# Kernel tuning notes

Measured on AMD Instinct MI355X. Metric: run time of the kernel, lower is better.

Reference implementation:

```python
import jax, jax.numpy as jnp
import numpy as np

N = 10000        # nodes
E = 320000       # edges (before self-loops)
F_IN = 128       # num_feature
H1, C1 = 16, 16  # GAT1: heads=16, out=16 -> concat 256
D = 256          # GAT2: heads=1, out=256
G = 64           # graphs in batch
L = 10           # num_label
NEG_SLOPE = 0.2


def setup_inputs() -> dict:
    key = jax.random.key(0)
    ks = jax.random.split(key, 13)
    sc = lambda f: 1.0 / np.sqrt(f)
    inp = {
        "x": jax.random.normal(ks[0], (N, F_IN), jnp.float32),
        "edge_index": jax.random.randint(ks[1], (2, E), 0, N, dtype=jnp.int32),
        "batch": jnp.sort(jax.random.randint(ks[2], (N,), 0, G, dtype=jnp.int32)),
        "W1": jax.random.normal(ks[3], (F_IN, H1 * C1), jnp.float32) * sc(F_IN),
        "a_src1": jax.random.normal(ks[4], (H1, C1), jnp.float32) * sc(C1),
        "a_dst1": jax.random.normal(ks[5], (H1, C1), jnp.float32) * sc(C1),
        "b1": jnp.zeros((H1 * C1,), jnp.float32),
        "W2": jax.random.normal(ks[6], (H1 * C1, D), jnp.float32) * sc(H1 * C1),
        "a_src2": jax.random.normal(ks[7], (1, D), jnp.float32) * sc(D),
        "a_dst2": jax.random.normal(ks[8], (1, D), jnp.float32) * sc(D),
        "b2": jnp.zeros((D,), jnp.float32),
        "lin_w": jax.random.normal(ks[9], (D, L), jnp.float32) * sc(D),
        "lin_b": jnp.zeros((L,), jnp.float32),
    }
    return inp


def _leaky(v):
    return jnp.where(v >= 0, v, NEG_SLOPE * v)


def gat_conv(x, src, dst, W, a_src, a_dst, bias, heads, ch):
    """PyG GATConv (eval mode): gather, leaky-relu logits, segment softmax over dst, scatter-add."""
    n = x.shape[0]
    h = (x @ W).reshape(n, heads, ch)                       # [N,H,C]
    al_s = jnp.sum(h * a_src, axis=-1)                      # [N,H]
    al_d = jnp.sum(h * a_dst, axis=-1)                      # [N,H]
    e = _leaky(al_s[src] + al_d[dst])                       # [Etot,H]
    m = jax.ops.segment_max(e, dst, num_segments=n)         # [N,H]
    m = jnp.where(jnp.isfinite(m), m, 0.0)
    ex = jnp.exp(e - m[dst])
    s = jax.ops.segment_sum(ex, dst, num_segments=n)        # [N,H] (>0: self-loops)
    alpha = ex / s[dst]                                     # [Etot,H]
    out = jax.ops.segment_sum(alpha[:, :, None] * h[src], dst, num_segments=n)
    return out.reshape(n, heads * ch) + bias


def reference(x, edge_index, batch, W1, a_src1, a_dst1, b1, W2, a_src2, a_dst2, b2, lin_w, lin_b):
    n = x.shape[0]
    loops = jnp.arange(n, dtype=edge_index.dtype)
    src = jnp.concatenate([edge_index[0], loops])           # add_self_loops=True (PyG default)
    dst = jnp.concatenate([edge_index[1], loops])

    h = gat_conv(x, src, dst, W1, a_src1, a_dst1, b1, H1, C1)
    h = jax.nn.relu(h)
    h = gat_conv(h, src, dst, W2, a_src2, a_dst2, b2, 1, D)

    # global_mean_pool over graph ids
    sums = jax.ops.segment_sum(h, batch, num_segments=G)    # [G,D]
    cnts = jax.ops.segment_sum(jnp.ones((n,), h.dtype), batch, num_segments=G)
    pooled = sums / jnp.maximum(cnts, 1.0)[:, None]

    # dropout is identity in eval mode
    return pooled @ lin_w + lin_b                           # [G,L]
```

## Files before the change

### kernel.cpp

```cpp
#include <hip/hip_runtime.h>
#include <hip/hip_bf16.h>
#include <math.h>

#define NEG_SLOPE 0.2f
#define LDS_FENCE() asm volatile("s_waitcnt lgkmcnt(0)" ::: "memory")

#define CSR_NB 128
#define CSR_CAP 2048

__device__ __forceinline__ ushort f2bf(float f) {
    uint x = __float_as_uint(f);
    x += 0x7fffu + ((x >> 16) & 1u);
    return (ushort)(x >> 16);
}
__device__ __forceinline__ float bf2f(ushort u) {
    return __uint_as_float((uint)u << 16);
}

template <int K, bool L1HEADS, bool XBF>
__device__ __forceinline__ void gemm_body(float* __restrict__ ws, int bx,
    const void* __restrict__ Xv, const float* __restrict__ W,
    ushort* __restrict__ Cb, const float* __restrict__ a_src,
    const float* __restrict__ a_dst, float* __restrict__ als,
    float* __restrict__ ald, int N) {
    int t = threadIdx.x;
    int lane = t & 63, wave = t >> 6;
    int n0 = bx * 16 + wave * 4;
    const size_t rowbytes = (size_t)K * (XBF ? 2 : 4);
    const char* Xr[4];
#pragma unroll
    for (int rr = 0; rr < 4; ++rr) {
        int r = min(n0 + rr, N - 1);
        Xr[rr] = (const char*)Xv + (size_t)__builtin_amdgcn_readfirstlane(r) * rowbytes;
    }
    float4 acc[4] = {};
    for (int kt = 0; kt < K; kt += 32) {
        const float4* Wg = (const float4*)(W + (size_t)kt * 256);
        float4* wsv = (float4*)ws;
#pragma unroll
        for (int i = 0; i < 8; ++i) wsv[t + i * 256] = Wg[t + i * 256];
        __syncthreads();
#pragma unroll 4
        for (int kk = 0; kk < 32; kk += 4) {
            int k = kt + kk;
            float4 w0 = *(const float4*)&ws[(size_t)(kk + 0) * 256 + lane * 4];
            float4 w1 = *(const float4*)&ws[(size_t)(kk + 1) * 256 + lane * 4];
            float4 w2 = *(const float4*)&ws[(size_t)(kk + 2) * 256 + lane * 4];
            float4 w3 = *(const float4*)&ws[(size_t)(kk + 3) * 256 + lane * 4];
#pragma unroll
            for (int rr = 0; rr < 4; ++rr) {
                float4 xv;
                if (XBF) {
                    ushort4 u = *(const ushort4*)(Xr[rr] + (size_t)k * 2);
                    xv.x = bf2f(u.x); xv.y = bf2f(u.y); xv.z = bf2f(u.z); xv.w = bf2f(u.w);
                } else {
                    xv = *(const float4*)(Xr[rr] + (size_t)k * 4);
                }
                acc[rr].x = fmaf(xv.x, w0.x, acc[rr].x);
                acc[rr].y = fmaf(xv.x, w0.y, acc[rr].y);
                acc[rr].z = fmaf(xv.x, w0.z, acc[rr].z);
                acc[rr].w = fmaf(xv.x, w0.w, acc[rr].w);
                acc[rr].x = fmaf(xv.y, w1.x, acc[rr].x);
                acc[rr].y = fmaf(xv.y, w1.y, acc[rr].y);
                acc[rr].z = fmaf(xv.y, w1.z, acc[rr].z);
                acc[rr].w = fmaf(xv.y, w1.w, acc[rr].w);
                acc[rr].x = fmaf(xv.z, w2.x, acc[rr].x);
                acc[rr].y = fmaf(xv.z, w2.y, acc[rr].y);
                acc[rr].z = fmaf(xv.z, w2.z, acc[rr].z);
                acc[rr].w = fmaf(xv.z, w2.w, acc[rr].w);
                acc[rr].x = fmaf(xv.w, w3.x, acc[rr].x);
                acc[rr].y = fmaf(xv.w, w3.y, acc[rr].y);
                acc[rr].z = fmaf(xv.w, w3.z, acc[rr].z);
                acc[rr].w = fmaf(xv.w, w3.w, acc[rr].w);
            }
        }
        __syncthreads();
    }
    if (n0 >= N) return;
    float4 asv = *(const float4*)(a_src + lane * 4);
    float4 adv = *(const float4*)(a_dst + lane * 4);
#pragma unroll
    for (int rr = 0; rr < 4; ++rr) {
        int n = n0 + rr;
        if (n >= N) break;
        ushort4 u;
        u.x = f2bf(acc[rr].x); u.y = f2bf(acc[rr].y);
        u.z = f2bf(acc[rr].z); u.w = f2bf(acc[rr].w);
        *(ushort4*)(Cb + (size_t)n * 256 + lane * 4) = u;
        float s = acc[rr].x * asv.x + acc[rr].y * asv.y + acc[rr].z * asv.z + acc[rr].w * asv.w;
        float d = acc[rr].x * adv.x + acc[rr].y * adv.y + acc[rr].z * adv.z + acc[rr].w * adv.w;
        if (L1HEADS) {
            s += __shfl_xor(s, 1); s += __shfl_xor(s, 2);
            d += __shfl_xor(d, 1); d += __shfl_xor(d, 2);
            if ((lane & 3) == 0) {
                als[n * 16 + (lane >> 2)] = s;
                ald[n * 16 + (lane >> 2)] = d;
            }
        } else {
#pragma unroll
            for (int off = 1; off <= 32; off <<= 1) {
                s += __shfl_xor(s, off);
                d += __shfl_xor(d, off);
            }
            if (lane == 0) { als[n] = s; ald[n] = d; }
        }
    }
}

__global__ __launch_bounds__(256) void k_scatter_gemm1(
    const int* __restrict__ ei, int E, int N, int NP, int CE,
    int* __restrict__ gcount, int* __restrict__ tmp,
    const float* __restrict__ X, const float* __restrict__ W1, ushort* __restrict__ A,
    const float* __restrict__ as1, const float* __restrict__ ad1,
    float* __restrict__ als1, float* __restrict__ ald1) {
    __shared__ float smem[32 * 256];
    if (blockIdx.x < CSR_NB) {
        int* lhist = (int*)smem;
        int t = threadIdx.x, b = blockIdx.x;
        for (int p = t; p < 384; p += 256) lhist[p] = 0;
        __syncthreads();
        int Etot = E + N;
        int e0 = b * CE, e1 = min(Etot, e0 + CE);
        for (int e = e0 + t; e < e1; e += 256) {
            int d = (e < E) ? ei[E + e] : (e - E);
            atomicAdd(&lhist[d >> 5], 1);
        }
        __syncthreads();
        for (int p = t; p < NP; p += 256) {
            int c = lhist[p];
            lhist[p] = c ? atomicAdd(&gcount[p], c) : 0;
        }
        __syncthreads();
        for (int e = e0 + t; e < e1; e += 256) {
            int s, d;
            if (e < E) { s = ei[e]; d = ei[E + e]; } else { s = d = e - E; }
            int p = d >> 5;
            int pos = atomicAdd(&lhist[p], 1);
            tmp[p * CSR_CAP + min(pos, CSR_CAP - 1)] = (s << 5) | (d & 31);
        }
    } else {
        gemm_body<128, true, false>(smem, blockIdx.x - CSR_NB, X, W1, A, as1, ad1, als1, ald1, N);
    }
}

__global__ __launch_bounds__(256) void k_gemm2(
    const ushort* __restrict__ Xb, const float* __restrict__ W, ushort* __restrict__ Cb,
    const float* __restrict__ as2, const float* __restrict__ ad2,
    float* __restrict__ als, float* __restrict__ ald, int N) {
    __shared__ float smem[32 * 256];
    gemm_body<256, false, true>(smem, blockIdx.x, Xb, W, Cb, as2, ad2, als, ald, N);
}

__global__ __launch_bounds__(256) void k_csr_final(const int* __restrict__ tmp,
                                                   const int* __restrict__ gcount,
                                                   int2* __restrict__ rowse,
                                                   int* __restrict__ col, int N) {
    __shared__ int dcnt[32], dcur[32];
    int t = threadIdx.x, p = blockIdx.x;
    int base = p * CSR_CAP;
    int cnt = min(gcount[p], CSR_CAP);
    if (t < 32) dcnt[t] = 0;
    __syncthreads();
    for (int i = t; i < cnt; i += 256) atomicAdd(&dcnt[tmp[base + i] & 31], 1);
    __syncthreads();
    if (t < 32) {
        int v = dcnt[t];
        int x = v;
#pragma unroll
        for (int off = 1; off < 32; off <<= 1) {
            int u = __shfl_up(x, off);
            if (t >= off) x += u;
        }
        int excl = x - v;
        dcur[t] = excl;
        int dst = (p << 5) + t;
        if (dst < N) rowse[dst] = make_int2(base + excl, base + excl + v);
    }
    __syncthreads();
    for (int i = t; i < cnt; i += 256) {
        int v = tmp[base + i];
        int pos = atomicAdd(&dcur[v & 31], 1);
        col[base + pos] = v >> 5;
    }
}

__global__ __launch_bounds__(256) void k_gather_h1(
    const int2* __restrict__ rowse, const int* __restrict__ col,
    const ushort* __restrict__ Hb, const float* __restrict__ als,
    const float* __restrict__ ald, const float* __restrict__ bias,
    ushort* __restrict__ outb, int N) {
    int wave = threadIdx.x >> 6, lane = threadIdx.x & 63;
    int n = blockIdx.x * 4 + wave;
    if (n >= N) return;
    int2 se2 = rowse[n];
    int start = se2.x, end = se2.y;
    float aldv = ald[n];
    float4 acc = {0.f, 0.f, 0.f, 0.f};
    float swsum = 0.f;
    const ushort* Hl = Hb + lane * 4;
    for (int base = start; base < end; base += 64) {
        int len = min(64, end - base);
        int s_r = 0;
        float w_r = 0.f;
        if (lane < len) {
            s_r = col[base + lane];
            float v = als[s_r] + aldv;
            v = v >= 0.f ? v : NEG_SLOPE * v;
            w_r = __expf(v);
        }
        swsum += w_r;
        int len8 = (len + 7) & ~7;
        for (int e = 0; e < len8; e += 8) {
            const ushort* hp[8];
            float we[8];
#pragma unroll
            for (int j = 0; j < 8; ++j) {
                hp[j] = Hl + (size_t)__shfl(s_r, e + j) * 256;
                we[j] = __shfl(w_r, e + j);
            }
            ushort4 uv[8];
#pragma unroll
            for (int j = 0; j < 8; ++j) uv[j] = *(const ushort4*)hp[j];
#pragma unroll
            for (int j = 0; j < 8; ++j) {
                acc.x = fmaf(we[j], bf2f(uv[j].x), acc.x);
                acc.y = fmaf(we[j], bf2f(uv[j].y), acc.y);
                acc.z = fmaf(we[j], bf2f(uv[j].z), acc.z);
                acc.w = fmaf(we[j], bf2f(uv[j].w), acc.w);
            }
        }
    }
#pragma unroll
    for (int off = 32; off >= 1; off >>= 1) swsum += __shfl_xor(swsum, off);
    float inv = 1.0f / swsum;
    float4 bv = *(const float4*)(bias + lane * 4);
    ushort4 o;
    o.x = f2bf(fmaf(acc.x, inv, bv.x));
    o.y = f2bf(fmaf(acc.y, inv, bv.y));
    o.z = f2bf(fmaf(acc.z, inv, bv.z));
    o.w = f2bf(fmaf(acc.w, inv, bv.w));
    *(ushort4*)(outb + (size_t)n * 256 + lane * 4) = o;
}

__global__ __launch_bounds__(256) void k_gather_h16(
    const int2* __restrict__ rowse, const int* __restrict__ col,
    const ushort* __restrict__ Hb, const float* __restrict__ als,
    const float* __restrict__ ald, const float* __restrict__ bias,
    ushort* __restrict__ outb, int N) {
    __shared__ float w_lds[4][64 * 16];
    int wave = threadIdx.x >> 6, lane = threadIdx.x & 63;
    int n = blockIdx.x * 4 + wave;
    if (n >= N) return;
    int2 se2 = rowse[n];
    int start = se2.x, end = se2.y;
    int hq = lane & 15;
    int eq = lane >> 4;
    float aldW = ald[n * 16 + hq];
    float4 acc = {0.f, 0.f, 0.f, 0.f};
    float swp = 0.f;
    const ushort* Hl = Hb + lane * 4;
    for (int base = start; base < end; base += 64) {
        int len = min(64, end - base);
        int s_r = (lane < len) ? col[base + lane] : 0;
#pragma unroll
        for (int k = 0; k < 16; ++k) {
            int esub = (k << 2) + eq;
            int s = __shfl(s_r, esub);
            float w = 0.f;
            if (esub < len) {
                float v = als[s * 16 + hq] + aldW;
                v = v >= 0.f ? v : NEG_SLOPE * v;
                w = __expf(v);
            }
            w_lds[wave][(esub << 4) + hq] = w;
            swp += w;
        }
        LDS_FENCE();
        int len8 = (len + 7) & ~7;
        for (int e = 0; e < len8; e += 8) {
            const ushort* hp[8];
            float we[8];
#pragma unroll
            for (int j = 0; j < 8; ++j) {
                hp[j] = Hl + (size_t)__shfl(s_r, e + j) * 256;
                we[j] = w_lds[wave][((e + j) << 4) + (lane >> 2)];
            }
            ushort4 uv[8];
#pragma unroll
            for (int j = 0; j < 8; ++j) uv[j] = *(const ushort4*)hp[j];
#pragma unroll
            for (int j = 0; j < 8; ++j) {
                acc.x = fmaf(we[j], bf2f(uv[j].x), acc.x);
                acc.y = fmaf(we[j], bf2f(uv[j].y), acc.y);
                acc.z = fmaf(we[j], bf2f(uv[j].z), acc.z);
                acc.w = fmaf(we[j], bf2f(uv[j].w), acc.w);
            }
        }
        LDS_FENCE();
    }
    swp += __shfl_xor(swp, 16);
    swp += __shfl_xor(swp, 32);
    float inv = 1.0f / __shfl(swp, lane >> 2);
    float4 bv = *(const float4*)(bias + lane * 4);
    ushort4 o;
    o.x = f2bf(fmaxf(fmaf(acc.x, inv, bv.x), 0.f));
    o.y = f2bf(fmaxf(fmaf(acc.y, inv, bv.y), 0.f));
    o.z = f2bf(fmaxf(fmaf(acc.z, inv, bv.z), 0.f));
    o.w = f2bf(fmaxf(fmaf(acc.w, inv, bv.w), 0.f));
    *(ushort4*)(outb + (size_t)n * 256 + lane * 4) = o;
}

__device__ __forceinline__ int lower_bound_i(const int* __restrict__ a, int n, int v) {
    int lo = 0, hi = n;
    while (lo < hi) {
        int mid = (lo + hi) >> 1;
        if (a[mid] < v) lo = mid + 1; else hi = mid;
    }
    return lo;
}

__global__ __launch_bounds__(1024) void k_pool_final(const ushort* __restrict__ Bb,
                                                     const int* __restrict__ batch,
                                                     const float* __restrict__ lw,
                                                     const float* __restrict__ lb,
                                                     float* __restrict__ out,
                                                     int N, int L) {
    __shared__ float psum[4][256];
    __shared__ float csum[256];
    int t = threadIdx.x;
    int c = t & 255, q = t >> 8;
    int g = blockIdx.x;
    int lo = lower_bound_i(batch, N, g);
    int hi = lower_bound_i(batch, N, g + 1);
    int len = hi - lo;
    int per = (len + 3) >> 2;
    int s0 = lo + q * per, s1 = min(hi, s0 + per);
    float acc = 0.f;
    for (int r = s0; r < s1; ++r) acc += bf2f(Bb[(size_t)r * 256 + c]);
    psum[q][c] = acc;
    __syncthreads();
    if (t < 256) csum[t] = psum[0][t] + psum[1][t] + psum[2][t] + psum[3][t];
    __syncthreads();
    int wave = t >> 6, lane = t & 63;
    if (wave < L) {
        int l = wave;
        float a = csum[lane] * lw[lane * L + l] +
                  csum[lane + 64] * lw[(lane + 64) * L + l] +
                  csum[lane + 128] * lw[(lane + 128) * L + l] +
                  csum[lane + 192] * lw[(lane + 192) * L + l];
#pragma unroll
        for (int off = 32; off >= 1; off >>= 1) a += __shfl_xor(a, off);
        if (lane == 0) out[g * L + l] = a / fmaxf((float)len, 1.0f) + lb[l];
    }
}

extern "C" void kernel_launch(void* const* d_in, const int* in_sizes, int n_in,
                              void* d_out, int out_size, void* d_ws, size_t ws_size,
                              hipStream_t stream) {
    const float* x   = (const float*)d_in[0];
    const int*   ei  = (const int*)d_in[1];
    const int*   bat = (const int*)d_in[2];
    const float* W1  = (const float*)d_in[3];
    const float* as1 = (const float*)d_in[4];
    const float* ad1 = (const float*)d_in[5];
    const float* b1  = (const float*)d_in[6];
    const float* W2  = (const float*)d_in[7];
    const float* as2 = (const float*)d_in[8];
    const float* ad2 = (const float*)d_in[9];
    const float* b2  = (const float*)d_in[10];
    const float* lw  = (const float*)d_in[11];
    const float* lb  = (const float*)d_in[12];
    float* out = (float*)d_out;

    const int N = in_sizes[2];
    const int E = in_sizes[1] / 2;
    const int G = 64, L = 10;
    const int Etot = E + N;
    const int NP = (N + 31) >> 5;
    const int CE = (Etot + CSR_NB - 1) / CSR_NB;

    float* A    = (float*)d_ws;
    float* B    = A + (size_t)N * 256;
    float* als1 = B + (size_t)N * 256;
    float* ald1 = als1 + (size_t)N * 16;
    float* als2 = ald1 + (size_t)N * 16;
    float* ald2 = als2 + N;
    int2* rowse = (int2*)(ald2 + N);
    int* col    = (int*)(rowse + N);
    int* tmp    = col + (size_t)NP * CSR_CAP;
    int* gcount = tmp + (size_t)NP * CSR_CAP;
    ushort* Abf = (ushort*)A;
    ushort* Bbf = (ushort*)B;

    const int BS = 256;
    auto nb = [](int n, int b) { return (n + b - 1) / b; };
    int nodes4 = nb(N, 4);
    int rows16 = nb(N, 16);

    hipMemsetAsync(gcount, 0, NP * sizeof(int), stream);
    k_scatter_gemm1<<<CSR_NB + rows16, BS, 0, stream>>>(ei, E, N, NP, CE, gcount, tmp,
                                                        x, W1, Abf, as1, ad1, als1, ald1);
    k_csr_final<<<NP, BS, 0, stream>>>(tmp, gcount, rowse, col, N);

    k_gather_h16<<<nodes4, BS, 0, stream>>>(rowse, col, Abf, als1, ald1, b1, Bbf, N);

    k_gemm2<<<rows16, BS, 0, stream>>>(Bbf, W2, Abf, as2, ad2, als2, ald2, N);
    k_gather_h1<<<nodes4, BS, 0, stream>>>(rowse, col, Abf, als2, ald2, b2, Bbf, N);

    k_pool_final<<<G, 1024, 0, stream>>>(Bbf, bat, lw, lb, out, N, L);
}
```

Before: 203.8 us.

## Use bf16 MFMA for second GAT GEMM with pre-transposed bf16 W2

```diff
diff --git a/kernel.cpp b/kernel.cpp
--- a/kernel.cpp
+++ b/kernel.cpp
@@ -7,6 +7,7 @@
 
 #define CSR_NB 128
 #define CSR_CAP 2048
+#define WT_NB 64
 
 __device__ __forceinline__ ushort f2bf(float f) {
     uint x = __float_as_uint(f);
@@ -17,21 +18,23 @@
     return __uint_as_float((uint)u << 16);
 }
 
-template <int K, bool L1HEADS, bool XBF>
-__device__ __forceinline__ void gemm_body(float* __restrict__ ws, int bx,
-    const void* __restrict__ Xv, const float* __restrict__ W,
+typedef __attribute__((ext_vector_type(8))) short bf16x8v;
+typedef __attribute__((ext_vector_type(4))) float f32x4;
+
+__device__ __forceinline__ void gemm1_body(float* __restrict__ ws, int bx,
+    const float* __restrict__ X, const float* __restrict__ W,
     ushort* __restrict__ Cb, const float* __restrict__ a_src,
     const float* __restrict__ a_dst, float* __restrict__ als,
     float* __restrict__ ald, int N) {
+    const int K = 128;
     int t = threadIdx.x;
     int lane = t & 63, wave = t >> 6;
     int n0 = bx * 16 + wave * 4;
-    const size_t rowbytes = (size_t)K * (XBF ? 2 : 4);
-    const char* Xr[4];
+    const float* Xr[4];
 #pragma unroll
     for (int rr = 0; rr < 4; ++rr) {
         int r = min(n0 + rr, N - 1);
-        Xr[rr] = (const char*)Xv + (size_t)__builtin_amdgcn_readfirstlane(r) * rowbytes;
+        Xr[rr] = X + (size_t)__builtin_amdgcn_readfirstlane(r) * K;
     }
     float4 acc[4] = {};
     for (int kt = 0; kt < K; kt += 32) {
@@ -49,13 +52,7 @@
             float4 w3 = *(const float4*)&ws[(size_t)(kk + 3) * 256 + lane * 4];
 #pragma unroll
             for (int rr = 0; rr < 4; ++rr) {
-                float4 xv;
-                if (XBF) {
-                    ushort4 u = *(const ushort4*)(Xr[rr] + (size_t)k * 2);
-                    xv.x = bf2f(u.x); xv.y = bf2f(u.y); xv.z = bf2f(u.z); xv.w = bf2f(u.w);
-                } else {
-                    xv = *(const float4*)(Xr[rr] + (size_t)k * 4);
-                }
+                float4 xv = *(const float4*)(Xr[rr] + k);
                 acc[rr].x = fmaf(xv.x, w0.x, acc[rr].x);
                 acc[rr].y = fmaf(xv.x, w0.y, acc[rr].y);
                 acc[rr].z = fmaf(xv.x, w0.z, acc[rr].z);
@@ -89,20 +86,11 @@
         *(ushort4*)(Cb + (size_t)n * 256 + lane * 4) = u;
         float s = acc[rr].x * asv.x + acc[rr].y * asv.y + acc[rr].z * asv.z + acc[rr].w * asv.w;
         float d = acc[rr].x * adv.x + acc[rr].y * adv.y + acc[rr].z * adv.z + acc[rr].w * adv.w;
-        if (L1HEADS) {
-            s += __shfl_xor(s, 1); s += __shfl_xor(s, 2);
-            d += __shfl_xor(d, 1); d += __shfl_xor(d, 2);
-            if ((lane & 3) == 0) {
-                als[n * 16 + (lane >> 2)] = s;
-                ald[n * 16 + (lane >> 2)] = d;
-            }
-        } else {
-#pragma unroll
-            for (int off = 1; off <= 32; off <<= 1) {
-                s += __shfl_xor(s, off);
-                d += __shfl_xor(d, off);
-            }
-            if (lane == 0) { als[n] = s; ald[n] = d; }
+        s += __shfl_xor(s, 1); s += __shfl_xor(s, 2);
+        d += __shfl_xor(d, 1); d += __shfl_xor(d, 2);
+        if ((lane & 3) == 0) {
+            als[n * 16 + (lane >> 2)] = s;
+            ald[n * 16 + (lane >> 2)] = d;
         }
     }
 }
@@ -112,11 +100,13 @@
     int* __restrict__ gcount, int* __restrict__ tmp,
     const float* __restrict__ X, const float* __restrict__ W1, ushort* __restrict__ A,
     const float* __restrict__ as1, const float* __restrict__ ad1,
-    float* __restrict__ als1, float* __restrict__ ald1) {
+    float* __restrict__ als1, float* __restrict__ ald1,
+    const float* __restrict__ W2, ushort* __restrict__ Wt) {
     __shared__ float smem[32 * 256];
+    int t = threadIdx.x;
     if (blockIdx.x < CSR_NB) {
         int* lhist = (int*)smem;
-        int t = threadIdx.x, b = blockIdx.x;
+        int b = blockIdx.x;
         for (int p = t; p < 384; p += 256) lhist[p] = 0;
         __syncthreads();
         int Etot = E + N;
@@ -138,17 +128,76 @@
             int pos = atomicAdd(&lhist[p], 1);
             tmp[p * CSR_CAP + min(pos, CSR_CAP - 1)] = (s << 5) | (d & 31);
         }
+    } else if (blockIdx.x < CSR_NB + WT_NB) {
+        float (*tile)[33] = (float (*)[33])smem;
+        int tb = blockIdx.x - CSR_NB;
+        int k0 = (tb >> 3) * 32, j0 = (tb & 7) * 32;
+        int c = t & 31, i0 = t >> 5;
+#pragma unroll
+        for (int p = 0; p < 4; ++p) {
+            int i = i0 + p * 8;
+            tile[i][c] = W2[(size_t)(k0 + i) * 256 + j0 + c];
+        }
+        __syncthreads();
+#pragma unroll
+        for (int p = 0; p < 4; ++p) {
+            int i = i0 + p * 8;
+            Wt[(size_t)(j0 + i) * 256 + k0 + c] = f2bf(tile[c][i]);
+        }
     } else {
-        gemm_body<128, true, false>(smem, blockIdx.x - CSR_NB, X, W1, A, as1, ad1, als1, ald1, N);
-    }
-}
-
-__global__ __launch_bounds__(256) void k_gemm2(
-    const ushort* __restrict__ Xb, const float* __restrict__ W, ushort* __restrict__ Cb,
-    const float* __restrict__ as2, const float* __restrict__ ad2,
-    float* __restrict__ als, float* __restrict__ ald, int N) {
-    __shared__ float smem[32 * 256];
-    gemm_body<256, false, true>(smem, blockIdx.x, Xb, W, Cb, as2, ad2, als, ald, N);
+        gemm1_body(smem, blockIdx.x - CSR_NB - WT_NB, X, W1, A, as1, ad1, als1, ald1, N);
+    }
+}
+
+__global__ __launch_bounds__(256) void k_gemm2_mfma(
+    const ushort* __restrict__ Xb, const ushort* __restrict__ Wt,
+    ushort* __restrict__ Cb, const float* __restrict__ as2,
+    const float* __restrict__ ad2, float* __restrict__ als,
+    float* __restrict__ ald, int N) {
+    __shared__ float red[4][16][2];
+    int t = threadIdx.x, lane = t & 63, w = t >> 6;
+    int n0 = blockIdx.x * 16;
+    int l15 = lane & 15, kb = lane >> 4;
+    int col0 = w * 64;
+    int arow = min(n0 + l15, N - 1);
+    const ushort* Xp = Xb + (size_t)arow * 256 + kb * 8;
+    f32x4 acc[4] = {f32x4{0,0,0,0}, f32x4{0,0,0,0}, f32x4{0,0,0,0}, f32x4{0,0,0,0}};
+#pragma unroll
+    for (int ks = 0; ks < 8; ++ks) {
+        bf16x8v a = *(const bf16x8v*)(Xp + ks * 32);
+#pragma unroll
+        for (int tt = 0; tt < 4; ++tt) {
+            const ushort* Bp = Wt + (size_t)(col0 + tt * 16 + l15) * 256 + ks * 32 + kb * 8;
+            bf16x8v b = *(const bf16x8v*)Bp;
+            acc[tt] = __builtin_amdgcn_mfma_f32_16x16x32_bf16(a, b, acc[tt], 0, 0, 0);
+        }
+    }
+#pragma unroll
+    for (int r = 0; r < 4; ++r) {
+        int n = n0 + kb * 4 + r;
+        float s = 0.f, d = 0.f;
+#pragma unroll
+        for (int tt = 0; tt < 4; ++tt) {
+            int col = col0 + tt * 16 + l15;
+            float v = acc[tt][r];
+            if (n < N) Cb[(size_t)n * 256 + col] = f2bf(v);
+            s += v * as2[col];
+            d += v * ad2[col];
+        }
+        s += __shfl_xor(s, 1); s += __shfl_xor(s, 2);
+        s += __shfl_xor(s, 4); s += __shfl_xor(s, 8);
+        d += __shfl_xor(d, 1); d += __shfl_xor(d, 2);
+        d += __shfl_xor(d, 4); d += __shfl_xor(d, 8);
+        if (l15 == 0) { red[w][kb * 4 + r][0] = s; red[w][kb * 4 + r][1] = d; }
+    }
+    __syncthreads();
+    if (t < 16) {
+        int n = n0 + t;
+        if (n < N) {
+            als[n] = red[0][t][0] + red[1][t][0] + red[2][t][0] + red[3][t][0];
+            ald[n] = red[0][t][1] + red[1][t][1] + red[2][t][1] + red[3][t][1];
+        }
+    }
 }
 
 __global__ __launch_bounds__(256) void k_csr_final(const int* __restrict__ tmp,
@@ -389,6 +438,7 @@
     int* col    = (int*)(rowse + N);
     int* tmp    = col + (size_t)NP * CSR_CAP;
     int* gcount = tmp + (size_t)NP * CSR_CAP;
+    ushort* Wt  = (ushort*)(gcount + NP);
     ushort* Abf = (ushort*)A;
     ushort* Bbf = (ushort*)B;
 
@@ -398,13 +448,13 @@
     int rows16 = nb(N, 16);
 
     hipMemsetAsync(gcount, 0, NP * sizeof(int), stream);
-    k_scatter_gemm1<<<CSR_NB + rows16, BS, 0, stream>>>(ei, E, N, NP, CE, gcount, tmp,
-                                                        x, W1, Abf, as1, ad1, als1, ald1);
+    k_scatter_gemm1<<<CSR_NB + WT_NB + rows16, BS, 0, stream>>>(
+        ei, E, N, NP, CE, gcount, tmp, x, W1, Abf, as1, ad1, als1, ald1, W2, Wt);
     k_csr_final<<<NP, BS, 0, stream>>>(tmp, gcount, rowse, col, N);
 
     k_gather_h16<<<nodes4, BS, 0, stream>>>(rowse, col, Abf, als1, ald1, b1, Bbf, N);
 
-    k_gemm2<<<rows16, BS, 0, stream>>>(Bbf, W2, Abf, as2, ad2, als2, ald2, N);
+    k_gemm2_mfma<<<rows16, BS, 0, stream>>>(Bbf, Wt, Abf, as2, ad2, als2, ald2, N);
     k_gather_h1<<<nodes4, BS, 0, stream>>>(rowse, col, Abf, als2, ald2, b2, Bbf, N);
 
     k_pool_final<<<G, 1024, 0, stream>>>(Bbf, bat, lw, lb, out, N, L);
```

Measured after the change: 191.5 us. 1.06x faster.
